# Kernel optimization log

Hardware: AMD Instinct MI355X
Metric: run time of the kernel (lower is better)

The kernel has to match this reference:

```python
import jax, jax.numpy as jnp
import numpy as np

EMBED_DIM = 1024


def setup_inputs() -> dict:
    key = jax.random.key(0)
    ks = jax.random.split(key, 9)
    d = EMBED_DIM
    s = 1.0 / np.sqrt(d)
    return {
        "x": jax.random.normal(ks[0], (4, 2048, d), dtype=jnp.float32),
        "wq": jax.random.normal(ks[1], (d, d), dtype=jnp.float32) * s,
        "bq": jnp.zeros((d,), dtype=jnp.float32),
        "wk": jax.random.normal(ks[2], (d, d), dtype=jnp.float32) * s,
        "bk": jnp.zeros((d,), dtype=jnp.float32),
        "wv": jax.random.normal(ks[3], (d, d), dtype=jnp.float32) * s,
        "bv": jnp.zeros((d,), dtype=jnp.float32),
        "wo": jax.random.normal(ks[4], (d, d), dtype=jnp.float32) * s,
        "bo": jnp.zeros((d,), dtype=jnp.float32),
    }


def reference(x, wq, bq, wk, bk, wv, bv, wo, bo):
    # x: [B, S, D]; weights stored as [D_in, D_out] (torch Linear applies x @ W.T,
    # here we fold the transpose into storage).
    d = x.shape[-1]
    q = x @ wq + bq
    k = x @ wk + bk
    v = x @ wv + bv
    scores = jnp.einsum('bqd,bkd->bqk', q, k) / jnp.sqrt(jnp.float32(d))
    attn = jax.nn.softmax(scores, axis=-1)
    out = jnp.einsum('bqk,bkd->bqd', attn, v)
    return out @ wo + bo
```

## Files before the change

### kernel.cpp

```cpp
#include <hip/hip_runtime.h>
#include <stdint.h>

typedef __attribute__((ext_vector_type(4))) float f32x4;
typedef __attribute__((ext_vector_type(8))) short short8v;
typedef __attribute__((ext_vector_type(4))) unsigned short ushort4v;
typedef __attribute__((ext_vector_type(8))) unsigned short ushort8v;

__device__ __forceinline__ unsigned short f2b(float x) {
  union { float f; unsigned int u; } c; c.f = x;
  unsigned int r = (c.u + 0x7fffu + ((c.u >> 16) & 1u)) >> 16;
  return (unsigned short)r;
}

__device__ __forceinline__ void gload_lds16(const void* g, void* l) {
  __builtin_amdgcn_global_load_lds(
      (const __attribute__((address_space(1))) void*)g,
      (__attribute__((address_space(3))) void*)l, 16, 0, 0);
}

__device__ __forceinline__ f32x4 MFMA16(short8v a, short8v b, f32x4 c) {
  return __builtin_amdgcn_mfma_f32_16x16x32_bf16(a, b, c, 0, 0, 0);
}

template <int N>
__device__ __forceinline__ void wvm() {
  if constexpr (N == 8) asm volatile("s_waitcnt vmcnt(8)" ::: "memory");
  else if constexpr (N == 6) asm volatile("s_waitcnt vmcnt(6)" ::: "memory");
  else if constexpr (N == 4) asm volatile("s_waitcnt vmcnt(4)" ::: "memory");
  else if constexpr (N == 3) asm volatile("s_waitcnt vmcnt(3)" ::: "memory");
  else asm volatile("s_waitcnt vmcnt(0)" ::: "memory");
}

__global__ __launch_bounds__(256) void cvt_bf16(const float* __restrict__ in,
                                                unsigned short* __restrict__ out,
                                                int n8) {
  for (int i = blockIdx.x * 256 + threadIdx.x; i < n8; i += gridDim.x * 256) {
    f32x4 a = *((const f32x4*)in + (size_t)i * 2);
    f32x4 b = *((const f32x4*)in + (size_t)i * 2 + 1);
    ushort8v o;
    o[0] = f2b(a[0]); o[1] = f2b(a[1]); o[2] = f2b(a[2]); o[3] = f2b(a[3]);
    o[4] = f2b(b[0]); o[5] = f2b(b[1]); o[6] = f2b(b[2]); o[7] = f2b(b[3]);
    *((ushort8v*)out + i) = o;
  }
}

__global__ __launch_bounds__(256) void wt4_bf16(const float* __restrict__ w0,
                                                const float* __restrict__ w1,
                                                const float* __restrict__ w2,
                                                const float* __restrict__ w3,
                                                unsigned short* __restrict__ o0,
                                                unsigned short* __restrict__ o1,
                                                unsigned short* __restrict__ o2,
                                                unsigned short* __restrict__ o3) {
  const int z = blockIdx.z;
  const float* W = z == 0 ? w0 : z == 1 ? w1 : z == 2 ? w2 : w3;
  unsigned short* WT = z == 0 ? o0 : z == 1 ? o1 : z == 2 ? o2 : o3;
  __shared__ float t[64][65];
  const int bi = blockIdx.y * 64, bj = blockIdx.x * 64;
#pragma unroll
  for (int i = 0; i < 16; ++i) {
    int idx = i * 256 + threadIdx.x;
    int r = idx >> 6, c = idx & 63;
    t[r][c] = W[(size_t)(bi + r) * 1024 + bj + c];
  }
  __syncthreads();
#pragma unroll
  for (int i = 0; i < 16; ++i) {
    int idx = i * 256 + threadIdx.x;
    int r = idx >> 6, c = idx & 63;
    WT[(size_t)(bj + r) * 1024 + bi + c] = f2b(t[c][r]);
  }
}

__global__ __launch_bounds__(256) void softmax_rows(float* __restrict__ S,
                                                    long long bstride) {
  float* row = S + (long long)blockIdx.y * bstride + (size_t)blockIdx.x * 2048;
  const int t = threadIdx.x;
  f32x4 a = *(const f32x4*)(row + t * 8);
  f32x4 b = *(const f32x4*)(row + t * 8 + 4);
  float m = fmaxf(fmaxf(fmaxf(a[0], a[1]), fmaxf(a[2], a[3])),
                  fmaxf(fmaxf(b[0], b[1]), fmaxf(b[2], b[3])));
#pragma unroll
  for (int o = 32; o; o >>= 1) m = fmaxf(m, __shfl_xor(m, o));
  __shared__ float red[4];
  const int wid = t >> 6, lane = t & 63;
  if (lane == 0) red[wid] = m;
  __syncthreads();
  m = fmaxf(fmaxf(red[0], red[1]), fmaxf(red[2], red[3]));
  float e[8];
  float s = 0.f;
#pragma unroll
  for (int j = 0; j < 4; ++j) { e[j] = __expf(a[j] - m); s += e[j]; }
#pragma unroll
  for (int j = 0; j < 4; ++j) { e[4 + j] = __expf(b[j] - m); s += e[4 + j]; }
#pragma unroll
  for (int o = 32; o; o >>= 1) s += __shfl_xor(s, o);
  __syncthreads();
  if (lane == 0) red[wid] = s;
  __syncthreads();
  s = red[0] + red[1] + red[2] + red[3];
  const float inv = 1.f / s;
  ushort8v o8;
#pragma unroll
  for (int j = 0; j < 8; ++j) o8[j] = f2b(e[j] * inv);
  __syncthreads();
  *((ushort8v*)row + t) = o8;
}

template <int EPI, int BM>
__global__ __launch_bounds__(512, 2) void gemm256(
    const unsigned short* __restrict__ A, int lda,
    const unsigned short* __restrict__ B, int ldb,
    void* __restrict__ C0, void* __restrict__ C1, void* __restrict__ C2,
    int ldc, const float* __restrict__ bias0, const float* __restrict__ bias1,
    const float* __restrict__ bias2, float scale, int K,
    long long bsA, long long bsB, long long bsC) {
  extern __shared__ __align__(16) char smem[];
  constexpr int ABY = BM * 64;
  constexpr int KHS = ABY + 16384;
  constexpr int SBUF = 2 * KHS;
  constexpr int MF = BM / 32;
  constexpr int FH = MF / 2;
  constexpr int AL = BM / 128;
  constexpr int L = AL + 2;

  const int tid = threadIdx.x;
  const int z = blockIdx.z;
  A += (long long)z * bsA;
  B += (long long)z * bsB;
  const int blkrow = blockIdx.y * BM, blkcol = blockIdx.x * 256;
  const int lane = tid & 63, wid = tid >> 6;
  const int kblk = lane >> 4, l15 = lane & 15;
  const int arw = (wid >> 2) * (BM / 2) + l15;
  const int brw = (wid & 3) * 64 + l15;
  const int aoff = arw * 64 + ((kblk ^ ((arw >> 1) & 3)) << 4);
  const int boff = ABY + brw * 64 + ((kblk ^ ((brw >> 1) & 3)) << 4);
  const int srow = tid >> 2;
  const int scc = (((tid & 3) ^ ((srow >> 1) & 3)) << 3);
  const unsigned short* ag = A + (size_t)(blkrow + srow) * lda + scc;
  const unsigned short* bg = B + (size_t)(blkcol + srow) * ldb + scc;

  auto stA = [&](char* buf, int kt, int kh) {
    const unsigned short* g = ag + kt * 64 + kh * 32;
    char* l = buf + kh * KHS + tid * 16;
#pragma unroll
    for (int rr = 0; rr < AL; ++rr)
      gload_lds16(g + (size_t)(rr * 128) * lda, l + rr * 8192);
  };
  auto stB = [&](char* buf, int kt, int kh) {
    const unsigned short* g = bg + kt * 64 + kh * 32;
    char* l = buf + ABY + kh * KHS + tid * 16;
    gload_lds16(g, l);
    gload_lds16(g + (size_t)128 * ldb, l + 8192);
  };

  f32x4 acc[MF][4] = {};
  short8v af[4], bf[4];

#define LDAH(BUF, KK, MB)                                                     \
  { _Pragma("unroll") for (int m_ = 0; m_ < FH; ++m_)                         \
      af[m_] = *(const short8v*)((BUF) + (KK)*KHS + aoff + ((MB) + m_) * 1024); }
#define LDB4(BUF, KK)                                                         \
  { _Pragma("unroll") for (int n_ = 0; n_ < 4; ++n_)                          \
      bf[n_] = *(const short8v*)((BUF) + (KK)*KHS + boff + n_ * 1024); }
#define MMH(MH)                                                               \
  { _Pragma("unroll") for (int m_ = 0; m_ < FH; ++m_)                         \
      _Pragma("unroll") for (int n_ = 0; n_ < 4; ++n_)                        \
        acc[(MH)*FH + m_][n_] = MFMA16(af[m_], bf[n_], acc[(MH)*FH + m_][n_]); }
#define BAR __builtin_amdgcn_s_barrier()
#define WLGKM0 asm volatile("s_waitcnt lgkmcnt(0)" ::: "memory")

  const int NT = K >> 6;
  stA(smem, 0, 0); stB(smem, 0, 0); stA(smem, 0, 1); stB(smem, 0, 1);
  wvm<L>();
  BAR;
  for (int t = 0; t < NT; ++t) {
    char* cur = smem + (t & 1) * SBUF;
    char* nxt = smem + ((t + 1) & 1) * SBUF;
    const bool pf = (t + 1 < NT);
    LDAH(cur, 0, 0);
    LDB4(cur, 0);
    if (pf) { stA(nxt, t + 1, 0); stB(nxt, t + 1, 0); }
    BAR; WLGKM0;
    __builtin_amdgcn_s_setprio(1);
    MMH(0);
    __builtin_amdgcn_s_setprio(0);
    BAR;
    LDAH(cur, 0, FH);
    if (pf) { stA(nxt, t + 1, 1); stB(nxt, t + 1, 1); }
    BAR; WLGKM0;
    __builtin_amdgcn_s_setprio(1);
    MMH(1);
    __builtin_amdgcn_s_setprio(0);
    if (pf) wvm<2 * L>(); else wvm<0>();
    BAR;
    LDAH(cur, 1, 0);
    LDB4(cur, 1);
    BAR; WLGKM0;
    __builtin_amdgcn_s_setprio(1);
    MMH(0);
    __builtin_amdgcn_s_setprio(0);
    BAR;
    LDAH(cur, 1, FH);
    BAR; WLGKM0;
    __builtin_amdgcn_s_setprio(1);
    MMH(1);
    __builtin_amdgcn_s_setprio(0);
    if (pf) wvm<L>();
    BAR;
  }

  const int gr0 = blkrow + (wid >> 2) * (BM / 2) + kblk * 4;
  const int gc0 = blkcol + (wid & 3) * 64 + l15;
  if (EPI == 0) {
    float* C = (float*)C0 + (long long)z * bsC;
#pragma unroll
    for (int mi = 0; mi < MF; ++mi)
#pragma unroll
      for (int n = 0; n < 4; ++n) {
        const int gc = gc0 + n * 16;
        const float badd = bias0 ? bias0[gc] : 0.f;
#pragma unroll
        for (int j = 0; j < 4; ++j)
          C[(size_t)(gr0 + mi * 16 + j) * ldc + gc] = acc[mi][n][j] * scale + badd;
      }
  } else if (EPI == 1) {
    unsigned short* C = (unsigned short*)C0 + (long long)z * bsC;
#pragma unroll
    for (int mi = 0; mi < MF; ++mi)
#pragma unroll
      for (int n = 0; n < 4; ++n) {
        const int gc = gc0 + n * 16;
        const float badd = bias0 ? bias0[gc] : 0.f;
#pragma unroll
        for (int j = 0; j < 4; ++j)
          C[(size_t)(gr0 + mi * 16 + j) * ldc + gc] = f2b(acc[mi][n][j] * scale + badd);
      }
  } else {
    const int seg = blkcol >> 10;
#pragma unroll
    for (int mi = 0; mi < MF; ++mi)
#pragma unroll
      for (int n = 0; n < 4; ++n) {
        const int gc = gc0 + n * 16;
        const int lc = gc - seg * 1024;
        if (seg < 2) {
          unsigned short* O = (unsigned short*)(seg == 0 ? C0 : C1);
          const float* bb = (seg == 0 ? bias0 : bias1);
          const float badd = bb[lc];
#pragma unroll
          for (int j = 0; j < 4; ++j)
            O[(size_t)(gr0 + mi * 16 + j) * 1024 + lc] = f2b(acc[mi][n][j] + badd);
        } else {
          unsigned short* O = (unsigned short*)C2;
          const float badd = bias2[lc];
          ushort4v pk;
#pragma unroll
          for (int j = 0; j < 4; ++j) pk[j] = f2b(acc[mi][n][j] + badd);
          *(ushort4v*)(O + (size_t)lc * 8192 + gr0 + mi * 16) = pk;
        }
      }
  }
#undef LDAH
#undef LDB4
#undef MMH
#undef BAR
#undef WLGKM0
}

template <int OMODE, bool BIAS, bool SCALE>
__global__ __launch_bounds__(256, 2) void gemm_bt(
    const unsigned short* __restrict__ A, int lda,
    const unsigned short* __restrict__ B, int ldb,
    void* __restrict__ Cp, int ldc,
    const float* __restrict__ bias, float scale, int K,
    long long bsA, long long bsB, long long bsC) {
  __shared__ unsigned short As[128 * 32];
  __shared__ unsigned short Bs[128 * 32];
  const int tid = threadIdx.x;
  A += (long long)blockIdx.z * bsA;
  B += (long long)blockIdx.z * bsB;
  const int brow = blockIdx.y * 128, bcol = blockIdx.x * 128;
  const int wid = tid >> 6, lane = tid & 63;
  const int wr = (wid >> 1) * 64, wc = (wid & 1) * 64;
  const int lrow = lane & 15, kblk = lane >> 4;
  f32x4 acc[4][4] = {};
  for (int kk = 0; kk < K; kk += 32) {
#pragma unroll
    for (int r = 0; r < 2; ++r) {
      int idx = r * 256 + tid;
      int row = idx >> 2, seg = (idx & 3) * 8;
      gload_lds16(A + (size_t)(brow + row) * lda + kk + seg, (char*)As + idx * 16);
      gload_lds16(B + (size_t)(bcol + row) * ldb + kk + seg, (char*)Bs + idx * 16);
    }
    __syncthreads();
    short8v af[4], bv[4];
#pragma unroll
    for (int m = 0; m < 4; ++m)
      af[m] = *(const short8v*)(As + (wr + m * 16 + lrow) * 32 + kblk * 8);
#pragma unroll
    for (int n = 0; n < 4; ++n)
      bv[n] = *(const short8v*)(Bs + (wc + n * 16 + lrow) * 32 + kblk * 8);
#pragma unroll
    for (int m = 0; m < 4; ++m)
#pragma unroll
      for (int n = 0; n < 4; ++n)
        acc[m][n] = MFMA16(af[m], bv[n], acc[m][n]);
    __syncthreads();
  }
  const int r0 = brow + wr + kblk * 4;
  const int c0 = bcol + wc + lrow;
  if (OMODE == 0) {
    float* C = (float*)Cp + (long long)blockIdx.z * bsC;
#pragma unroll
    for (int m = 0; m < 4; ++m)
#pragma unroll
      for (int n = 0; n < 4; ++n) {
        const int cc = c0 + n * 16;
        const float badd = BIAS ? bias[cc] : 0.f;
#pragma unroll
        for (int j = 0; j < 4; ++j) {
          float v = acc[m][n][j];
          if (SCALE) v *= scale;
          C[(size_t)(r0 + m * 16 + j) * ldc + cc] = v + badd;
        }
      }
  } else if (OMODE == 1) {
    unsigned short* C = (unsigned short*)Cp + (long long)blockIdx.z * bsC;
#pragma unroll
    for (int m = 0; m < 4; ++m)
#pragma unroll
      for (int n = 0; n < 4; ++n) {
        const int cc = c0 + n * 16;
        const float badd = BIAS ? bias[cc] : 0.f;
#pragma unroll
        for (int j = 0; j < 4; ++j) {
          float v = acc[m][n][j];
          if (SCALE) v *= scale;
          C[(size_t)(r0 + m * 16 + j) * ldc + cc] = f2b(v + badd);
        }
      }
  } else {
    unsigned short* C = (unsigned short*)Cp + (long long)blockIdx.z * bsC;
#pragma unroll
    for (int m = 0; m < 4; ++m)
#pragma unroll
      for (int n = 0; n < 4; ++n) {
        const int cc = c0 + n * 16;
        const float badd = BIAS ? bias[cc] : 0.f;
        ushort4v pk;
#pragma unroll
        for (int j = 0; j < 4; ++j) {
          float v = acc[m][n][j];
          if (SCALE) v *= scale;
          pk[j] = f2b(v + badd);
        }
        *(ushort4v*)(C + (size_t)cc * ldc + (r0 + m * 16)) = pk;
      }
  }
}

extern "C" void kernel_launch(void* const* d_in, const int* in_sizes, int n_in,
                              void* d_out, int out_size, void* d_ws, size_t ws_size,
                              hipStream_t stream) {
  const float* x  = (const float*)d_in[0];
  const float* wq = (const float*)d_in[1];
  const float* bq = (const float*)d_in[2];
  const float* wk = (const float*)d_in[3];
  const float* bk = (const float*)d_in[4];
  const float* wv = (const float*)d_in[5];
  const float* bv = (const float*)d_in[6];
  const float* wo = (const float*)d_in[7];
  const float* bo = (const float*)d_in[8];
  float* out = (float*)d_out;
  char* ws = (char*)d_ws;

  const long long WELEM = 1024LL * 1024;
  const long long BATCH = 2048LL * 1024;
  const long long FULL  = 4 * BATCH;
  const long long SELEM = 2048LL * 2048;

  const size_t need_A = 8388608ull + 5ull * 16777216 + 4ull * 16777216;
  const size_t need_C = 8388608ull + 4ull * 4194304 + 16777216ull;

  if (ws_size >= need_A) {
    unsigned short* wqT = (unsigned short*)ws;
    unsigned short* wkT = wqT + WELEM;
    unsigned short* wvT = wkT + WELEM;
    unsigned short* woT = wvT + WELEM;
    unsigned short* xb  = woT + WELEM;
    unsigned short* qb  = xb + FULL;
    unsigned short* kb  = qb + FULL;
    unsigned short* vt  = kb + FULL;
    unsigned short* ao  = vt + FULL;
    float* S = (float*)(ao + FULL);

    hipFuncSetAttribute(reinterpret_cast<const void*>(&gemm256<2, 256>),
                        hipFuncAttributeMaxDynamicSharedMemorySize, 131072);
    hipFuncSetAttribute(reinterpret_cast<const void*>(&gemm256<0, 256>),
                        hipFuncAttributeMaxDynamicSharedMemorySize, 131072);
    hipFuncSetAttribute(reinterpret_cast<const void*>(&gemm256<1, 128>),
                        hipFuncAttributeMaxDynamicSharedMemorySize, 98304);
    hipFuncSetAttribute(reinterpret_cast<const void*>(&gemm256<0, 128>),
                        hipFuncAttributeMaxDynamicSharedMemorySize, 98304);

    cvt_bf16<<<2048, 256, 0, stream>>>(x, xb, (int)(FULL / 8));
    wt4_bf16<<<dim3(16, 16, 4), 256, 0, stream>>>(wq, wk, wv, wo, wqT, wkT, wvT, woT);

    gemm256<2, 256><<<dim3(12, 32, 1), 512, 131072, stream>>>(
        xb, 1024, wqT, 1024, qb, kb, vt, 0, bq, bk, bv, 1.f, 1024, 0, 0, 0);
    gemm256<0, 256><<<dim3(8, 8, 4), 512, 131072, stream>>>(
        qb, 1024, kb, 1024, S, nullptr, nullptr, 2048, nullptr, nullptr,
        nullptr, 0.03125f, 1024, BATCH, BATCH, SELEM);
    softmax_rows<<<dim3(2048, 4), 256, 0, stream>>>(S, SELEM);
    gemm256<1, 128><<<dim3(4, 16, 4), 512, 98304, stream>>>(
        (const unsigned short*)S, 4096, vt, 8192, ao, nullptr, nullptr, 1024,
        nullptr, nullptr, nullptr, 1.f, 2048, 2 * SELEM, 2048, BATCH);
    gemm256<0, 128><<<dim3(4, 64, 1), 512, 98304, stream>>>(
        ao, 1024, woT, 1024, out, nullptr, nullptr, 1024, bo, nullptr, nullptr,
        1.f, 1024, 0, 0, 0);
  } else if (ws_size >= need_C) {
    unsigned short* wqT = (unsigned short*)ws;
    unsigned short* wkT = wqT + WELEM;
    unsigned short* wvT = wkT + WELEM;
    unsigned short* woT = wvT + WELEM;
    unsigned short* xb  = woT + WELEM;
    unsigned short* qb  = xb + BATCH;
    unsigned short* kb  = qb + BATCH;
    unsigned short* vtb = kb + BATCH;
    float* S = (float*)(vtb + BATCH);

    wt4_bf16<<<dim3(16, 16, 4), 256, 0, stream>>>(wq, wk, wv, wo, wqT, wkT, wvT, woT);

    for (int b = 0; b < 4; ++b) {
      cvt_bf16<<<1024, 256, 0, stream>>>(x + b * BATCH, xb, (int)(BATCH / 8));
      dim3 gqkv(8, 16);
      gemm_bt<1, true, false><<<gqkv, 256, 0, stream>>>(xb, 1024, wqT, 1024, qb, 1024, bq, 1.f, 1024, 0, 0, 0);
      gemm_bt<1, true, false><<<gqkv, 256, 0, stream>>>(xb, 1024, wkT, 1024, kb, 1024, bk, 1.f, 1024, 0, 0, 0);
      gemm_bt<2, true, false><<<gqkv, 256, 0, stream>>>(xb, 1024, wvT, 1024, vtb, 2048, bv, 1.f, 1024, 0, 0, 0);
      gemm_bt<0, false, true><<<dim3(16, 16), 256, 0, stream>>>(
          qb, 1024, kb, 1024, S, 2048, nullptr, 0.03125f, 1024, 0, 0, 0);
      softmax_rows<<<dim3(2048, 1), 256, 0, stream>>>(S, 0);
      gemm_bt<1, false, false><<<dim3(8, 16), 256, 0, stream>>>(
          (const unsigned short*)S, 4096, vtb, 2048, xb, 1024, nullptr, 1.f, 2048, 0, 0, 0);
      gemm_bt<0, true, false><<<dim3(8, 16), 256, 0, stream>>>(
          xb, 1024, woT, 1024, out + b * BATCH, 1024, bo, 1.f, 1024, 0, 0, 0);
    }
  }
}
```

Baseline: 229.5 us.

## Replace QKV projection GEMM with simple 128x128-tile single-buffered MFMA kernel

Swaps the fused QKV projection from the templated 256-row, 512-thread, double-buffered GEMM to a new 128x128-tile kernel with 256 threads, static LDS and a single K-stage of 32. The smaller tiles give more workgroups (24x64) and lower LDS use per block, which may raise occupancy. In exchange it loses pipelining of loads against MFMA, takes two barriers per K step, and writes Q/K outputs with scalar strided stores instead of the original epilogue.

```diff
diff --git a/kernel.cpp b/kernel.cpp
--- a/kernel.cpp
+++ b/kernel.cpp
@@ -105,6 +105,75 @@
   for (int j = 0; j < 8; ++j) o8[j] = f2b(e[j] * inv);
   __syncthreads();
   *((ushort8v*)row + t) = o8;
+}
+
+__global__ __launch_bounds__(256, 2) void gemm_qkv128(
+    const unsigned short* __restrict__ A,
+    const unsigned short* __restrict__ B,
+    unsigned short* __restrict__ Q, unsigned short* __restrict__ Kp,
+    unsigned short* __restrict__ Vt,
+    const float* __restrict__ bq, const float* __restrict__ bk,
+    const float* __restrict__ bv) {
+  __shared__ unsigned short As[128 * 32];
+  __shared__ unsigned short Bs[128 * 32];
+  const int tid = threadIdx.x;
+  const int brow = blockIdx.y * 128, bcol = blockIdx.x * 128;
+  const int wid = tid >> 6, lane = tid & 63;
+  const int wr = (wid >> 1) * 64, wc = (wid & 1) * 64;
+  const int lrow = lane & 15, kblk = lane >> 4;
+  f32x4 acc[4][4] = {};
+  for (int kk = 0; kk < 1024; kk += 32) {
+#pragma unroll
+    for (int r = 0; r < 2; ++r) {
+      int idx = r * 256 + tid;
+      int row = idx >> 2, seg = (idx & 3) * 8;
+      gload_lds16(A + (size_t)(brow + row) * 1024 + kk + seg, (char*)As + idx * 16);
+      gload_lds16(B + (size_t)(bcol + row) * 1024 + kk + seg, (char*)Bs + idx * 16);
+    }
+    __syncthreads();
+    short8v af[4], bf[4];
+#pragma unroll
+    for (int m = 0; m < 4; ++m)
+      af[m] = *(const short8v*)(As + (wr + m * 16 + lrow) * 32 + kblk * 8);
+#pragma unroll
+    for (int n = 0; n < 4; ++n)
+      bf[n] = *(const short8v*)(Bs + (wc + n * 16 + lrow) * 32 + kblk * 8);
+#pragma unroll
+    for (int m = 0; m < 4; ++m)
+#pragma unroll
+      for (int n = 0; n < 4; ++n)
+        acc[m][n] = MFMA16(af[m], bf[n], acc[m][n]);
+    __syncthreads();
+  }
+  const int r0 = brow + wr + kblk * 4;
+  const int c0 = bcol + wc + lrow;
+  const int seg = bcol >> 10;
+  if (seg < 2) {
+    unsigned short* O = seg == 0 ? Q : Kp;
+    const float* bb = seg == 0 ? bq : bk;
+#pragma unroll
+    for (int m = 0; m < 4; ++m)
+#pragma unroll
+      for (int n = 0; n < 4; ++n) {
+        const int lc = c0 + n * 16 - seg * 1024;
+        const float badd = bb[lc];
+#pragma unroll
+        for (int j = 0; j < 4; ++j)
+          O[(size_t)(r0 + m * 16 + j) * 1024 + lc] = f2b(acc[m][n][j] + badd);
+      }
+  } else {
+#pragma unroll
+    for (int m = 0; m < 4; ++m)
+#pragma unroll
+      for (int n = 0; n < 4; ++n) {
+        const int lc = c0 + n * 16 - 2048;
+        const float badd = bv[lc];
+        ushort4v pk;
+#pragma unroll
+        for (int j = 0; j < 4; ++j) pk[j] = f2b(acc[m][n][j] + badd);
+        *(ushort4v*)(Vt + (size_t)lc * 8192 + r0 + m * 16) = pk;
+      }
+  }
 }
 
 template <int EPI, int BM>
@@ -395,8 +464,6 @@
     unsigned short* ao  = vt + FULL;
     float* S = (float*)(ao + FULL);
 
-    hipFuncSetAttribute(reinterpret_cast<const void*>(&gemm256<2, 256>),
-                        hipFuncAttributeMaxDynamicSharedMemorySize, 131072);
     hipFuncSetAttribute(reinterpret_cast<const void*>(&gemm256<0, 256>),
                         hipFuncAttributeMaxDynamicSharedMemorySize, 131072);
     hipFuncSetAttribute(reinterpret_cast<const void*>(&gemm256<1, 128>),
@@ -407,8 +474,8 @@
     cvt_bf16<<<2048, 256, 0, stream>>>(x, xb, (int)(FULL / 8));
     wt4_bf16<<<dim3(16, 16, 4), 256, 0, stream>>>(wq, wk, wv, wo, wqT, wkT, wvT, woT);
 
-    gemm256<2, 256><<<dim3(12, 32, 1), 512, 131072, stream>>>(
-        xb, 1024, wqT, 1024, qb, kb, vt, 0, bq, bk, bv, 1.f, 1024, 0, 0, 0);
+    gemm_qkv128<<<dim3(24, 64), 256, 0, stream>>>(
+        xb, wqT, qb, kb, vt, bq, bk, bv);
     gemm256<0, 256><<<dim3(8, 8, 4), 512, 131072, stream>>>(
         qb, 1024, kb, 1024, S, nullptr, nullptr, 2048, nullptr, nullptr,
         nullptr, 0.03125f, 1024, BATCH, BATCH, SELEM);
```

After: 212.9 us. 7.2% less time.

## Use triple-buffered 128x256 GEMM and store attention scores in bf16

Applied to the files above, without the earlier changes.

Replaces the two-phase double-buffered gemm256 with a single 128x256-tile GEMM that keeps three LDS stages, prefetches two k-tiles ahead, and uses one barrier per k-step with an 8-way XOR swizzle. The QK^T GEMM now writes bf16 scores instead of fp32, and a new bf16 softmax works in place. This halves score-matrix traffic and is meant to reduce barrier stalls. The cost is more LDS per block, which may limit occupancy, and scores rounded to bf16 before softmax, which loses precision.

```diff
diff --git a/kernel.cpp b/kernel.cpp
--- a/kernel.cpp
+++ b/kernel.cpp
@@ -12,6 +12,11 @@
   return (unsigned short)r;
 }
 
+__device__ __forceinline__ float b2f(unsigned short x) {
+  union { unsigned int u; float f; } c; c.u = ((unsigned int)x) << 16;
+  return c.f;
+}
+
 __device__ __forceinline__ void gload_lds16(const void* g, void* l) {
   __builtin_amdgcn_global_load_lds(
       (const __attribute__((address_space(1))) void*)g,
@@ -20,15 +25,6 @@
 
 __device__ __forceinline__ f32x4 MFMA16(short8v a, short8v b, f32x4 c) {
   return __builtin_amdgcn_mfma_f32_16x16x32_bf16(a, b, c, 0, 0, 0);
-}
-
-template <int N>
-__device__ __forceinline__ void wvm() {
-  if constexpr (N == 8) asm volatile("s_waitcnt vmcnt(8)" ::: "memory");
-  else if constexpr (N == 6) asm volatile("s_waitcnt vmcnt(6)" ::: "memory");
-  else if constexpr (N == 4) asm volatile("s_waitcnt vmcnt(4)" ::: "memory");
-  else if constexpr (N == 3) asm volatile("s_waitcnt vmcnt(3)" ::: "memory");
-  else asm volatile("s_waitcnt vmcnt(0)" ::: "memory");
 }
 
 __global__ __launch_bounds__(256) void cvt_bf16(const float* __restrict__ in,
@@ -72,6 +68,40 @@
   }
 }
 
+__global__ __launch_bounds__(256) void softmax_bf16(unsigned short* __restrict__ S,
+                                                    long long bstride) {
+  unsigned short* row = S + (long long)blockIdx.y * bstride + (size_t)blockIdx.x * 2048;
+  const int t = threadIdx.x;
+  ushort8v u = *((const ushort8v*)row + t);
+  float v[8];
+#pragma unroll
+  for (int j = 0; j < 8; ++j) v[j] = b2f(u[j]);
+  float m = v[0];
+#pragma unroll
+  for (int j = 1; j < 8; ++j) m = fmaxf(m, v[j]);
+#pragma unroll
+  for (int o = 32; o; o >>= 1) m = fmaxf(m, __shfl_xor(m, o));
+  __shared__ float red[4];
+  const int wid = t >> 6, lane = t & 63;
+  if (lane == 0) red[wid] = m;
+  __syncthreads();
+  m = fmaxf(fmaxf(red[0], red[1]), fmaxf(red[2], red[3]));
+  float s = 0.f;
+#pragma unroll
+  for (int j = 0; j < 8; ++j) { v[j] = __expf(v[j] - m); s += v[j]; }
+#pragma unroll
+  for (int o = 32; o; o >>= 1) s += __shfl_xor(s, o);
+  __syncthreads();
+  if (lane == 0) red[wid] = s;
+  __syncthreads();
+  s = red[0] + red[1] + red[2] + red[3];
+  const float inv = 1.f / s;
+  ushort8v o8;
+#pragma unroll
+  for (int j = 0; j < 8; ++j) o8[j] = f2b(v[j] * inv);
+  *((ushort8v*)row + t) = o8;
+}
+
 __global__ __launch_bounds__(256) void softmax_rows(float* __restrict__ S,
                                                     long long bstride) {
   float* row = S + (long long)blockIdx.y * bstride + (size_t)blockIdx.x * 2048;
@@ -107,8 +137,8 @@
   *((ushort8v*)row + t) = o8;
 }
 
-template <int EPI, int BM>
-__global__ __launch_bounds__(512, 2) void gemm256(
+template <int EPI>
+__global__ __launch_bounds__(512, 2) void gemm128x256(
     const unsigned short* __restrict__ A, int lda,
     const unsigned short* __restrict__ B, int ldb,
     void* __restrict__ C0, void* __restrict__ C1, void* __restrict__ C2,
@@ -116,130 +146,105 @@
     const float* __restrict__ bias2, float scale, int K,
     long long bsA, long long bsB, long long bsC) {
   extern __shared__ __align__(16) char smem[];
-  constexpr int ABY = BM * 64;
-  constexpr int KHS = ABY + 16384;
-  constexpr int SBUF = 2 * KHS;
-  constexpr int MF = BM / 32;
-  constexpr int FH = MF / 2;
-  constexpr int AL = BM / 128;
-  constexpr int L = AL + 2;
+  constexpr int TSZ = 49152;
 
   const int tid = threadIdx.x;
   const int z = blockIdx.z;
   A += (long long)z * bsA;
   B += (long long)z * bsB;
-  const int blkrow = blockIdx.y * BM, blkcol = blockIdx.x * 256;
+  const int blkrow = blockIdx.y * 128, blkcol = blockIdx.x * 256;
   const int lane = tid & 63, wid = tid >> 6;
   const int kblk = lane >> 4, l15 = lane & 15;
-  const int arw = (wid >> 2) * (BM / 2) + l15;
-  const int brw = (wid & 3) * 64 + l15;
-  const int aoff = arw * 64 + ((kblk ^ ((arw >> 1) & 3)) << 4);
-  const int boff = ABY + brw * 64 + ((kblk ^ ((brw >> 1) & 3)) << 4);
-  const int srow = tid >> 2;
-  const int scc = (((tid & 3) ^ ((srow >> 1) & 3)) << 3);
-  const unsigned short* ag = A + (size_t)(blkrow + srow) * lda + scc;
-  const unsigned short* bg = B + (size_t)(blkcol + srow) * ldb + scc;
-
-  auto stA = [&](char* buf, int kt, int kh) {
-    const unsigned short* g = ag + kt * 64 + kh * 32;
-    char* l = buf + kh * KHS + tid * 16;
-#pragma unroll
-    for (int rr = 0; rr < AL; ++rr)
-      gload_lds16(g + (size_t)(rr * 128) * lda, l + rr * 8192);
+  const int wr = (wid >> 2) * 64, wc = (wid & 3) * 64;
+  const int sw = l15 & 7;
+
+  const int srow = tid >> 3;
+  const int scol = ((tid & 7) ^ (srow & 7)) << 3;
+  const unsigned short* ag = A + (size_t)(blkrow + srow) * lda + scol;
+  const unsigned short* bg = B + (size_t)(blkcol + srow) * ldb + scol;
+  const int ldsoff = tid * 16;
+
+  auto stage = [&](char* buf, int kt) {
+    const unsigned short* a0 = ag + kt * 64;
+    const unsigned short* b0 = bg + kt * 64;
+    gload_lds16(a0, buf + ldsoff);
+    gload_lds16(a0 + (size_t)64 * lda, buf + 8192 + ldsoff);
+    gload_lds16(b0, buf + 16384 + ldsoff);
+    gload_lds16(b0 + (size_t)64 * ldb, buf + 24576 + ldsoff);
+    gload_lds16(b0 + (size_t)128 * ldb, buf + 32768 + ldsoff);
+    gload_lds16(b0 + (size_t)192 * ldb, buf + 40960 + ldsoff);
   };
-  auto stB = [&](char* buf, int kt, int kh) {
-    const unsigned short* g = bg + kt * 64 + kh * 32;
-    char* l = buf + ABY + kh * KHS + tid * 16;
-    gload_lds16(g, l);
-    gload_lds16(g + (size_t)128 * ldb, l + 8192);
-  };
-
-  f32x4 acc[MF][4] = {};
-  short8v af[4], bf[4];
-
-#define LDAH(BUF, KK, MB)                                                     \
-  { _Pragma("unroll") for (int m_ = 0; m_ < FH; ++m_)                         \
-      af[m_] = *(const short8v*)((BUF) + (KK)*KHS + aoff + ((MB) + m_) * 1024); }
-#define LDB4(BUF, KK)                                                         \
-  { _Pragma("unroll") for (int n_ = 0; n_ < 4; ++n_)                          \
-      bf[n_] = *(const short8v*)((BUF) + (KK)*KHS + boff + n_ * 1024); }
-#define MMH(MH)                                                               \
-  { _Pragma("unroll") for (int m_ = 0; m_ < FH; ++m_)                         \
-      _Pragma("unroll") for (int n_ = 0; n_ < 4; ++n_)                        \
-        acc[(MH)*FH + m_][n_] = MFMA16(af[m_], bf[n_], acc[(MH)*FH + m_][n_]); }
-#define BAR __builtin_amdgcn_s_barrier()
-#define WLGKM0 asm volatile("s_waitcnt lgkmcnt(0)" ::: "memory")
-
+
+  f32x4 acc[4][4] = {};
   const int NT = K >> 6;
-  stA(smem, 0, 0); stB(smem, 0, 0); stA(smem, 0, 1); stB(smem, 0, 1);
-  wvm<L>();
-  BAR;
+
+  stage(smem, 0);
+  stage(smem + TSZ, 1);
+  asm volatile("s_waitcnt vmcnt(6)" ::: "memory");
+  __builtin_amdgcn_s_barrier();
+
+  char* rb = smem;
+  char* sb = smem + 2 * TSZ;
   for (int t = 0; t < NT; ++t) {
-    char* cur = smem + (t & 1) * SBUF;
-    char* nxt = smem + ((t + 1) & 1) * SBUF;
-    const bool pf = (t + 1 < NT);
-    LDAH(cur, 0, 0);
-    LDB4(cur, 0);
-    if (pf) { stA(nxt, t + 1, 0); stB(nxt, t + 1, 0); }
-    BAR; WLGKM0;
-    __builtin_amdgcn_s_setprio(1);
-    MMH(0);
-    __builtin_amdgcn_s_setprio(0);
-    BAR;
-    LDAH(cur, 0, FH);
-    if (pf) { stA(nxt, t + 1, 1); stB(nxt, t + 1, 1); }
-    BAR; WLGKM0;
-    __builtin_amdgcn_s_setprio(1);
-    MMH(1);
-    __builtin_amdgcn_s_setprio(0);
-    if (pf) wvm<2 * L>(); else wvm<0>();
-    BAR;
-    LDAH(cur, 1, 0);
-    LDB4(cur, 1);
-    BAR; WLGKM0;
-    __builtin_amdgcn_s_setprio(1);
-    MMH(0);
-    __builtin_amdgcn_s_setprio(0);
-    BAR;
-    LDAH(cur, 1, FH);
-    BAR; WLGKM0;
-    __builtin_amdgcn_s_setprio(1);
-    MMH(1);
-    __builtin_amdgcn_s_setprio(0);
-    if (pf) wvm<L>();
-    BAR;
-  }
-
-  const int gr0 = blkrow + (wid >> 2) * (BM / 2) + kblk * 4;
-  const int gc0 = blkcol + (wid & 3) * 64 + l15;
+    if (t + 2 < NT) stage(sb, t + 2);
+    short8v af[4], bf[4];
+#pragma unroll
+    for (int ks = 0; ks < 2; ++ks) {
+      const int kc = ks * 4 + kblk;
+      const int sc = (kc ^ sw) << 4;
+#pragma unroll
+      for (int m = 0; m < 4; ++m)
+        af[m] = *(const short8v*)(rb + (wr + m * 16 + l15) * 128 + sc);
+#pragma unroll
+      for (int n = 0; n < 4; ++n)
+        bf[n] = *(const short8v*)(rb + 16384 + (wc + n * 16 + l15) * 128 + sc);
+      __builtin_amdgcn_s_setprio(1);
+#pragma unroll
+      for (int m = 0; m < 4; ++m)
+#pragma unroll
+        for (int n = 0; n < 4; ++n)
+          acc[m][n] = MFMA16(af[m], bf[n], acc[m][n]);
+      __builtin_amdgcn_s_setprio(0);
+    }
+    if (t + 1 < NT) {
+      if (t + 2 < NT) asm volatile("s_waitcnt vmcnt(6)" ::: "memory");
+      else            asm volatile("s_waitcnt vmcnt(0)" ::: "memory");
+      __builtin_amdgcn_s_barrier();
+    }
+    rb += TSZ; if (rb == smem + 3 * TSZ) rb = smem;
+    sb += TSZ; if (sb == smem + 3 * TSZ) sb = smem;
+  }
+
+  const int gr0 = blkrow + wr + kblk * 4;
+  const int gc0 = blkcol + wc + l15;
   if (EPI == 0) {
     float* C = (float*)C0 + (long long)z * bsC;
 #pragma unroll
-    for (int mi = 0; mi < MF; ++mi)
+    for (int m = 0; m < 4; ++m)
 #pragma unroll
       for (int n = 0; n < 4; ++n) {
         const int gc = gc0 + n * 16;
         const float badd = bias0 ? bias0[gc] : 0.f;
 #pragma unroll
         for (int j = 0; j < 4; ++j)
-          C[(size_t)(gr0 + mi * 16 + j) * ldc + gc] = acc[mi][n][j] * scale + badd;
+          C[(size_t)(gr0 + m * 16 + j) * ldc + gc] = acc[m][n][j] * scale + badd;
       }
   } else if (EPI == 1) {
     unsigned short* C = (unsigned short*)C0 + (long long)z * bsC;
 #pragma unroll
-    for (int mi = 0; mi < MF; ++mi)
+    for (int m = 0; m < 4; ++m)
 #pragma unroll
       for (int n = 0; n < 4; ++n) {
         const int gc = gc0 + n * 16;
         const float badd = bias0 ? bias0[gc] : 0.f;
 #pragma unroll
         for (int j = 0; j < 4; ++j)
-          C[(size_t)(gr0 + mi * 16 + j) * ldc + gc] = f2b(acc[mi][n][j] * scale + badd);
+          C[(size_t)(gr0 + m * 16 + j) * ldc + gc] = f2b(acc[m][n][j] * scale + badd);
       }
   } else {
     const int seg = blkcol >> 10;
 #pragma unroll
-    for (int mi = 0; mi < MF; ++mi)
+    for (int m = 0; m < 4; ++m)
 #pragma unroll
       for (int n = 0; n < 4; ++n) {
         const int gc = gc0 + n * 16;
@@ -250,22 +255,17 @@
           const float badd = bb[lc];
 #pragma unroll
           for (int j = 0; j < 4; ++j)
-            O[(size_t)(gr0 + mi * 16 + j) * 1024 + lc] = f2b(acc[mi][n][j] + badd);
+            O[(size_t)(gr0 + m * 16 + j) * 1024 + lc] = f2b(acc[m][n][j] + badd);
         } else {
           unsigned short* O = (unsigned short*)C2;
           const float badd = bias2[lc];
           ushort4v pk;
 #pragma unroll
-          for (int j = 0; j < 4; ++j) pk[j] = f2b(acc[mi][n][j] + badd);
-          *(ushort4v*)(O + (size_t)lc * 8192 + gr0 + mi * 16) = pk;
+          for (int j = 0; j < 4; ++j) pk[j] = f2b(acc[m][n][j] + badd);
+          *(ushort4v*)(O + (size_t)lc * 8192 + gr0 + m * 16) = pk;
         }
       }
   }
-#undef LDAH
-#undef LDB4
-#undef MMH
-#undef BAR
-#undef WLGKM0
 }
 
 template <int OMODE, bool BIAS, bool SCALE>
@@ -393,30 +393,28 @@
     unsigned short* kb  = qb + FULL;
     unsigned short* vt  = kb + FULL;
     unsigned short* ao  = vt + FULL;
-    float* S = (float*)(ao + FULL);
-
-    hipFuncSetAttribute(reinterpret_cast<const void*>(&gemm256<2, 256>),
-                        hipFuncAttributeMaxDynamicSharedMemorySize, 131072);
-    hipFuncSetAttribute(reinterpret_cast<const void*>(&gemm256<0, 256>),
-                        hipFuncAttributeMaxDynamicSharedMemorySize, 131072);
-    hipFuncSetAttribute(reinterpret_cast<const void*>(&gemm256<1, 128>),
-                        hipFuncAttributeMaxDynamicSharedMemorySize, 98304);
-    hipFuncSetAttribute(reinterpret_cast<const void*>(&gemm256<0, 128>),
-                        hipFuncAttributeMaxDynamicSharedMemorySize, 98304);
+    unsigned short* S   = ao + FULL;
+
+    hipFuncSetAttribute(reinterpret_cast<const void*>(&gemm128x256<0>),
+                        hipFuncAttributeMaxDynamicSharedMemorySize, 147456);
+    hipFuncSetAttribute(reinterpret_cast<const void*>(&gemm128x256<1>),
+                        hipFuncAttributeMaxDynamicSharedMemorySize, 147456);
+    hipFuncSetAttribute(reinterpret_cast<const void*>(&gemm128x256<2>),
+                        hipFuncAttributeMaxDynamicSharedMemorySize, 147456);
 
     cvt_bf16<<<2048, 256, 0, stream>>>(x, xb, (int)(FULL / 8));
     wt4_bf16<<<dim3(16, 16, 4), 256, 0, stream>>>(wq, wk, wv, wo, wqT, wkT, wvT, woT);
 
-    gemm256<2, 256><<<dim3(12, 32, 1), 512, 131072, stream>>>(
+    gemm128x256<2><<<dim3(12, 64, 1), 512, 147456, stream>>>(
         xb, 1024, wqT, 1024, qb, kb, vt, 0, bq, bk, bv, 1.f, 1024, 0, 0, 0);
-    gemm256<0, 256><<<dim3(8, 8, 4), 512, 131072, stream>>>(
+    gemm128x256<1><<<dim3(8, 16, 4), 512, 147456, stream>>>(
         qb, 1024, kb, 1024, S, nullptr, nullptr, 2048, nullptr, nullptr,
         nullptr, 0.03125f, 1024, BATCH, BATCH, SELEM);
-    softmax_rows<<<dim3(2048, 4), 256, 0, stream>>>(S, SELEM);
-    gemm256<1, 128><<<dim3(4, 16, 4), 512, 98304, stream>>>(
-        (const unsigned short*)S, 4096, vt, 8192, ao, nullptr, nullptr, 1024,
-        nullptr, nullptr, nullptr, 1.f, 2048, 2 * SELEM, 2048, BATCH);
-    gemm256<0, 128><<<dim3(4, 64, 1), 512, 98304, stream>>>(
+    softmax_bf16<<<dim3(2048, 4), 256, 0, stream>>>(S, SELEM);
+    gemm128x256<1><<<dim3(4, 16, 4), 512, 147456, stream>>>(
+        S, 2048, vt, 8192, ao, nullptr, nullptr, 1024,
+        nullptr, nullptr, nullptr, 1.f, 2048, SELEM, 2048, BATCH);
+    gemm128x256<0><<<dim3(4, 64, 1), 512, 147456, stream>>>(
         ao, 1024, woT, 1024, out, nullptr, nullptr, 1024, bo, nullptr, nullptr,
         1.f, 1024, 0, 0, 0);
   } else if (ws_size >= need_C) {
```

Measured after the change: 198.9 us. 13.3% less time.
